# Optimization experiments

Measured on AMD Instinct MI355X. Metric: run time of the kernel, lower is better.

The kernel has to match this reference:

```python
import jax, jax.numpy as jnp
import numpy as np


def setup_inputs() -> dict:
    key = jax.random.key(0)
    k1, k2 = jax.random.split(key)
    N1, N2, C, W, H = 128, 128, 768, 16, 16
    x = jax.random.normal(k1, (N1, C, W, H), dtype=jnp.float32)
    y = jax.random.normal(k2, (N2, C, W, H), dtype=jnp.float32)
    return {"x": x, "y": y}


def reference(x, y):
    """NNGPKernel.forward with y given, diag=False, and the abstract
    propagate() taken as identity. Computes the initial ConvKP tensors:
      xy[n1*N2+n2, 0, w, h] = mean_c x[n1,c,w,h] * y[n2,c,w,h]
      xx[n1, 0, w, h]       = mean_c x[n1,c,w,h]**2
      yy[n2, 0, w, h]       = mean_c y[n2,c,w,h]**2
    The pairwise channel-mean is expressed as a batched contraction over c
    (per spatial location), avoiding the O(N1*N2*C*W*H) broadcast intermediate
    of the original torch code.
    """
    N1, C, W, H = x.shape
    N2 = y.shape[0]
    inv_c = jnp.asarray(1.0 / C, dtype=x.dtype)
    # [N1, N2, W, H] pairwise channel correlation, then flatten pair dims
    xy = (jnp.einsum('ncwh,mcwh->nmwh', x, y) * inv_c).reshape(N1 * N2, 1, W, H)
    xx = jnp.mean(x * x, axis=1, keepdims=True)  # [N1, 1, W, H]
    yy = jnp.mean(y * y, axis=1, keepdims=True)  # [N2, 1, W, H]
    return xy, xx, yy
```

## Files before the change

### kernel.cpp

```cpp
#include <hip/hip_runtime.h>

#define AS1 __attribute__((address_space(1)))
#define AS3 __attribute__((address_space(3)))

typedef float f32x4 __attribute__((ext_vector_type(4)));
typedef long lx2 __attribute__((ext_vector_type(2)));

static constexpr int C = 768;
static constexpr int NB = 128;
static constexpr int S  = 256;
static constexpr int XY_ELEMS  = NB * NB * S;
static constexpr int XSQ_ELEMS = NB * S;
static constexpr size_t WS_TENSOR_B = (size_t)S * NB * C;

__global__ __launch_bounds__(256) void pass1(const float* __restrict__ x,
                                             const float* __restrict__ y,
                                             unsigned char* __restrict__ xb,
                                             unsigned char* __restrict__ yb,
                                             float* __restrict__ out) {
  const int b      = blockIdx.x;
  const int tensor = b >> 10;
  const int local  = b & 1023;
  const int n      = local >> 3;
  const int st     = (local >> 1) & 3;
  const int ch2    = local & 1;

  const float*   src = tensor ? y  : x;
  unsigned char* dst = tensor ? yb : xb;
  float*         sqo = out + XY_ELEMS + tensor * XSQ_ELEMS;

  __shared__ float tile[2][32 * 68];

  const int t  = threadIdx.x;
  const int cl = t >> 4;
  const int s4 = (t & 15) * 4;
  const int sl = t >> 2;
  const int cq = t & 3;
  const int sn = (n >> 1) & 3;

  const float* srcn =
      src + (size_t)n * (C * S) + (size_t)(ch2 * 384) * S + st * 64;
  unsigned char* dstrow = dst + ((size_t)(st * 64 + sl) * NB + n) * C;

  f32x4 acc = {0.f, 0.f, 0.f, 0.f};
  f32x4 c0r, c1r, n0r, n1r;

  c0r = __builtin_nontemporal_load(
      reinterpret_cast<const f32x4*>(srcn + (size_t)cl * S + s4));
  c1r = __builtin_nontemporal_load(
      reinterpret_cast<const f32x4*>(srcn + (size_t)(16 + cl) * S + s4));

#pragma unroll
  for (int ch = 0; ch < 12; ++ch) {
    float* tb = tile[ch & 1];

    if (ch < 11) {
      const float* p0 = srcn + (size_t)((ch + 1) * 32 + cl) * S + s4;
      const float* p1 = srcn + (size_t)((ch + 1) * 32 + 16 + cl) * S + s4;
      n0r = __builtin_nontemporal_load(reinterpret_cast<const f32x4*>(p0));
      n1r = __builtin_nontemporal_load(reinterpret_cast<const f32x4*>(p1));
    }

    acc += c0r * c0r;
    acc += c1r * c1r;
    *reinterpret_cast<f32x4*>(
        &tb[cl * 68 + (s4 ^ (((cl >> 3) & 3) << 3))]) = c0r;
    *reinterpret_cast<f32x4*>(
        &tb[(16 + cl) * 68 + (s4 ^ ((((16 + cl) >> 3) & 3) << 3))]) = c1r;

    asm volatile("s_waitcnt lgkmcnt(0)" ::: "memory");
    __builtin_amdgcn_s_barrier();

    float f[8];
#pragma unroll
    for (int i = 0; i < 8; ++i)
      f[i] = tb[(cq * 8 + i) * 68 + (sl ^ (cq << 3))];
    int lo = __builtin_amdgcn_cvt_pk_fp8_f32(f[0], f[1], 0, false);
    lo     = __builtin_amdgcn_cvt_pk_fp8_f32(f[2], f[3], lo, true);
    int hi = __builtin_amdgcn_cvt_pk_fp8_f32(f[4], f[5], 0, false);
    hi     = __builtin_amdgcn_cvt_pk_fp8_f32(f[6], f[7], hi, true);
    uint2 v8 = make_uint2((unsigned)lo, (unsigned)hi);

    const int kt   = ch2 * 6 + (ch >> 1);
    const int slot = 2 * (cq ^ sn) + (ch & 1);
    *reinterpret_cast<uint2*>(dstrow + kt * 64 + slot * 8) = v8;

    c0r = n0r;
    c1r = n1r;
  }

  __syncthreads();
  float* part = &tile[0][0];
#pragma unroll
  for (int j = 0; j < 4; ++j) part[cl * 64 + s4 + j] = acc[j];
  __syncthreads();
  if (t < 64) {
    float ssum = 0.f;
#pragma unroll
    for (int i = 0; i < 16; ++i) ssum += part[i * 64 + t];
    atomicAdd(&sqo[n * S + st * 64 + t], ssum * (1.0f / 768.0f));
  }
}

__global__ __launch_bounds__(256) void pass2(const unsigned char* __restrict__ xb,
                                             const unsigned char* __restrict__ yb,
                                             float* __restrict__ ws2) {
  const int bid = blockIdx.x;
  const int s = ((bid & 7) << 5) | (bid >> 3);

  const unsigned char* A = xb + (size_t)s * (NB * C);
  const unsigned char* B = yb + (size_t)s * (NB * C);

  __shared__ unsigned char As[2][128 * 64];
  __shared__ unsigned char Bs[2][128 * 64];

  const int t    = threadIdx.x;
  const int lane = t & 63;
  const int w    = t >> 6;
  const int wn   = w >> 1;
  const int wm   = w & 1;

  const unsigned char* gA[2];
  const unsigned char* gB[2];
  int lo16[2];
#pragma unroll
  for (int i = 0; i < 2; ++i) {
    int ci  = i * 256 + t;
    int row = ci >> 2;
    int j16 = ci & 3;
    gA[i]   = A + row * C + j16 * 16;
    gB[i]   = B + row * C + j16 * 16;
    lo16[i] = ci * 16;
  }

#define STAGE(K0, BUF)                                                        \
  {                                                                           \
    _Pragma("unroll") for (int i = 0; i < 2; ++i) {                           \
      __builtin_amdgcn_global_load_lds(                                       \
          (const AS1 unsigned int*)(gA[i] + (K0)*64),                         \
          (AS3 unsigned int*)((char*)As[BUF] + lo16[i]), 16, 0, 0);           \
      __builtin_amdgcn_global_load_lds(                                       \
          (const AS1 unsigned int*)(gB[i] + (K0)*64),                         \
          (AS3 unsigned int*)((char*)Bs[BUF] + lo16[i]), 16, 0, 0);           \
    }                                                                         \
  }

  f32x4 acc[4][4] = {};

  STAGE(0, 0);

#pragma unroll
  for (int k0 = 0; k0 < 12; ++k0) {
    if (k0 < 11) STAGE(k0 + 1, (k0 + 1) & 1);

    if (k0 < 11) {
      asm volatile("s_waitcnt vmcnt(4)" ::: "memory");
    } else {
      asm volatile("s_waitcnt vmcnt(0)" ::: "memory");
    }
    __builtin_amdgcn_s_barrier();

    const char* Ab = (const char*)As[k0 & 1];
    const char* Bb = (const char*)Bs[k0 & 1];

    lx2 av[4], bv[4];
    const int q = lane >> 4;
#pragma unroll
    for (int mi = 0; mi < 4; ++mi) {
      int row = wn * 64 + mi * 16 + (lane & 15);
      av[mi] = *reinterpret_cast<const lx2*>(
          Ab + row * 64 + ((q ^ ((row >> 1) & 3)) * 16));
    }
#pragma unroll
    for (int nj = 0; nj < 4; ++nj) {
      int row = wm * 64 + nj * 16 + (lane & 15);
      bv[nj] = *reinterpret_cast<const lx2*>(
          Bb + row * 64 + ((q ^ ((row >> 1) & 3)) * 16));
    }
#pragma unroll
    for (int mi = 0; mi < 4; ++mi)
#pragma unroll
      for (int nj = 0; nj < 4; ++nj) {
        acc[mi][nj] = __builtin_amdgcn_mfma_f32_16x16x32_fp8_fp8(
            av[mi][0], bv[nj][0], acc[mi][nj], 0, 0, 0);
        acc[mi][nj] = __builtin_amdgcn_mfma_f32_16x16x32_fp8_fp8(
            av[mi][1], bv[nj][1], acc[mi][nj], 0, 0, 0);
      }

    if (k0 < 11) __builtin_amdgcn_s_barrier();
  }
#undef STAGE

  const float inv = 1.0f / 768.0f;
  float* w2 = ws2 + (size_t)s * (NB * NB);
#pragma unroll
  for (int mi = 0; mi < 4; ++mi) {
#pragma unroll
    for (int nj = 0; nj < 4; ++nj) {
      f32x4 v = acc[mi][nj] * inv;
      int mm = wm * 64 + nj * 16 + (lane & 15);
      int nn = wn * 64 + mi * 16 + (lane >> 4) * 4;
      *reinterpret_cast<f32x4*>(w2 + (size_t)mm * NB + nn) = v;
    }
  }
}

__global__ __launch_bounds__(256) void pass3(const float* __restrict__ ws2,
                                             float* __restrict__ out) {
  const int bid = blockIdx.x;
  const int m   = bid & 127;
  const int st  = (bid >> 7) & 3;
  const int nt  = bid >> 9;
  const int t   = threadIdx.x;
  const int l16 = t & 15;
  const int hi4 = t >> 4;

  __shared__ float tile[64 * 64];

  const float* src = ws2 + ((size_t)(st * 64) * NB + m) * NB + nt * 64;
#pragma unroll
  for (int i = 0; i < 4; ++i) {
    int s_local = hi4 + 16 * i;
    f32x4 v = *reinterpret_cast<const f32x4*>(
        src + (size_t)s_local * (NB * NB) + l16 * 4);
    int chunk = l16 ^ ((s_local >> 2) & 15);
    *reinterpret_cast<f32x4*>(&tile[s_local * 64 + chunk * 4]) = v;
  }
  __syncthreads();

  float* dst = out + ((size_t)(nt * 64) * NB + m) * S + st * 64;
#pragma unroll
  for (int i = 0; i < 4; ++i) {
    int n_local = hi4 + 16 * i;
    int cb      = (n_local >> 2) & 15;
    int ne      = n_local & 3;
    int s4      = l16 * 4;
    f32x4 v;
#pragma unroll
    for (int j = 0; j < 4; ++j) {
      int ss = s4 + j;
      v[j] = tile[ss * 64 + ((cb ^ ((ss >> 2) & 15)) << 2) + ne];
    }
    __builtin_nontemporal_store(
        v, reinterpret_cast<f32x4*>(dst + (size_t)n_local * (NB * S) + s4));
  }
}

extern "C" void kernel_launch(void* const* d_in, const int* in_sizes, int n_in,
                              void* d_out, int out_size, void* d_ws, size_t ws_size,
                              hipStream_t stream) {
  const float* x = (const float*)d_in[0];
  const float* y = (const float*)d_in[1];
  float* out = (float*)d_out;

  unsigned char* xb = (unsigned char*)d_ws;
  unsigned char* yb = xb + WS_TENSOR_B;
  float* ws2 = (float*)((char*)d_ws + 2 * WS_TENSOR_B);

  hipMemsetAsync(out + XY_ELEMS, 0, (size_t)2 * XSQ_ELEMS * sizeof(float),
                 stream);
  pass1<<<2048, 256, 0, stream>>>(x, y, xb, yb, out);
  pass2<<<256, 256, 0, stream>>>(xb, yb, ws2);
  pass3<<<1024, 256, 0, stream>>>(ws2, out);
}
```

Baseline: 84.04 us.

## Restructure fp8 quantize pass to full-row spatial tiles with per-thread square sums

Rewrites the first pass so each block covers all 256 spatial positions of a 128-channel slice, with one thread per spatial location. Each thread reads 16 channels per step from shared memory, accumulates the squared-sum itself, and writes 16 bytes of fp8. This removes the cross-thread partial-sum reduction and its extra barriers, and each block issues one atomic per spatial location per channel chunk. The cost is a grid of 1536 blocks instead of 2048, more loads in flight per thread, and unpadded shared-memory tiles whose column reads could hit bank conflicts.

```diff
diff --git a/kernel.cpp b/kernel.cpp
--- a/kernel.cpp
+++ b/kernel.cpp
@@ -19,87 +19,82 @@
                                              unsigned char* __restrict__ yb,
                                              float* __restrict__ out) {
   const int b      = blockIdx.x;
-  const int tensor = b >> 10;
-  const int local  = b & 1023;
-  const int n      = local >> 3;
-  const int st     = (local >> 1) & 3;
-  const int ch2    = local & 1;
+  const int tensor = b / 768;
+  const int local  = b - tensor * 768;
+  const int n      = local / 6;
+  const int cr     = local - n * 6;
 
   const float*   src = tensor ? y  : x;
   unsigned char* dst = tensor ? yb : xb;
   float*         sqo = out + XY_ELEMS + tensor * XSQ_ELEMS;
 
-  __shared__ float tile[2][32 * 68];
-
-  const int t  = threadIdx.x;
-  const int cl = t >> 4;
-  const int s4 = (t & 15) * 4;
-  const int sl = t >> 2;
-  const int cq = t & 3;
-  const int sn = (n >> 1) & 3;
-
-  const float* srcn =
-      src + (size_t)n * (C * S) + (size_t)(ch2 * 384) * S + st * 64;
-  unsigned char* dstrow = dst + ((size_t)(st * 64 + sl) * NB + n) * C;
-
-  f32x4 acc = {0.f, 0.f, 0.f, 0.f};
-  f32x4 c0r, c1r, n0r, n1r;
-
-  c0r = __builtin_nontemporal_load(
-      reinterpret_cast<const f32x4*>(srcn + (size_t)cl * S + s4));
-  c1r = __builtin_nontemporal_load(
-      reinterpret_cast<const f32x4*>(srcn + (size_t)(16 + cl) * S + s4));
-
-#pragma unroll
-  for (int ch = 0; ch < 12; ++ch) {
+  __shared__ float tile[2][16 * 256];
+
+  const int t    = threadIdx.x;
+  const int w    = t >> 6;
+  const int lane = t & 63;
+  const int sn   = (n >> 1) & 3;
+
+  const float* srcn = src + (size_t)n * (C * S) + (size_t)(cr * 128) * S;
+  unsigned char* dstrow = dst + ((size_t)t * NB + n) * C;
+
+  float sq = 0.f;
+  f32x4 cur[4], nxt[4];
+
+#pragma unroll
+  for (int i = 0; i < 4; ++i)
+    cur[i] = __builtin_nontemporal_load(reinterpret_cast<const f32x4*>(
+        srcn + (size_t)(i * 4 + w) * S + lane * 4));
+
+#pragma unroll
+  for (int ch = 0; ch < 8; ++ch) {
     float* tb = tile[ch & 1];
 
-    if (ch < 11) {
-      const float* p0 = srcn + (size_t)((ch + 1) * 32 + cl) * S + s4;
-      const float* p1 = srcn + (size_t)((ch + 1) * 32 + 16 + cl) * S + s4;
-      n0r = __builtin_nontemporal_load(reinterpret_cast<const f32x4*>(p0));
-      n1r = __builtin_nontemporal_load(reinterpret_cast<const f32x4*>(p1));
-    }
-
-    acc += c0r * c0r;
-    acc += c1r * c1r;
-    *reinterpret_cast<f32x4*>(
-        &tb[cl * 68 + (s4 ^ (((cl >> 3) & 3) << 3))]) = c0r;
-    *reinterpret_cast<f32x4*>(
-        &tb[(16 + cl) * 68 + (s4 ^ ((((16 + cl) >> 3) & 3) << 3))]) = c1r;
+    if (ch < 7) {
+#pragma unroll
+      for (int i = 0; i < 4; ++i)
+        nxt[i] = __builtin_nontemporal_load(reinterpret_cast<const f32x4*>(
+            srcn + (size_t)((ch + 1) * 16 + i * 4 + w) * S + lane * 4));
+    }
+
+#pragma unroll
+    for (int i = 0; i < 4; ++i)
+      *reinterpret_cast<f32x4*>(&tb[(i * 4 + w) * 256 + lane * 4]) = cur[i];
 
     asm volatile("s_waitcnt lgkmcnt(0)" ::: "memory");
     __builtin_amdgcn_s_barrier();
 
-    float f[8];
-#pragma unroll
-    for (int i = 0; i < 8; ++i)
-      f[i] = tb[(cq * 8 + i) * 68 + (sl ^ (cq << 3))];
-    int lo = __builtin_amdgcn_cvt_pk_fp8_f32(f[0], f[1], 0, false);
-    lo     = __builtin_amdgcn_cvt_pk_fp8_f32(f[2], f[3], lo, true);
-    int hi = __builtin_amdgcn_cvt_pk_fp8_f32(f[4], f[5], 0, false);
-    hi     = __builtin_amdgcn_cvt_pk_fp8_f32(f[6], f[7], hi, true);
-    uint2 v8 = make_uint2((unsigned)lo, (unsigned)hi);
-
-    const int kt   = ch2 * 6 + (ch >> 1);
-    const int slot = 2 * (cq ^ sn) + (ch & 1);
-    *reinterpret_cast<uint2*>(dstrow + kt * 64 + slot * 8) = v8;
-
-    c0r = n0r;
-    c1r = n1r;
-  }
-
-  __syncthreads();
-  float* part = &tile[0][0];
-#pragma unroll
-  for (int j = 0; j < 4; ++j) part[cl * 64 + s4 + j] = acc[j];
-  __syncthreads();
-  if (t < 64) {
-    float ssum = 0.f;
-#pragma unroll
-    for (int i = 0; i < 16; ++i) ssum += part[i * 64 + t];
-    atomicAdd(&sqo[n * S + st * 64 + t], ssum * (1.0f / 768.0f));
-  }
+    float f[16];
+#pragma unroll
+    for (int i = 0; i < 16; ++i) f[i] = tb[i * 256 + t];
+#pragma unroll
+    for (int i = 0; i < 16; ++i) sq += f[i] * f[i];
+
+    int w0 = __builtin_amdgcn_cvt_pk_fp8_f32(f[0], f[1], 0, false);
+    w0     = __builtin_amdgcn_cvt_pk_fp8_f32(f[2], f[3], w0, true);
+    int w1 = __builtin_amdgcn_cvt_pk_fp8_f32(f[4], f[5], 0, false);
+    w1     = __builtin_amdgcn_cvt_pk_fp8_f32(f[6], f[7], w1, true);
+    int w2 = __builtin_amdgcn_cvt_pk_fp8_f32(f[8], f[9], 0, false);
+    w2     = __builtin_amdgcn_cvt_pk_fp8_f32(f[10], f[11], w2, true);
+    int w3 = __builtin_amdgcn_cvt_pk_fp8_f32(f[12], f[13], 0, false);
+    w3     = __builtin_amdgcn_cvt_pk_fp8_f32(f[14], f[15], w3, true);
+
+    const int c0 = cr * 128 + ch * 16;
+    const int kt = c0 >> 6;
+    const int u0 = (c0 >> 3) & 7;
+    const int s0 = 2 * ((u0 & 3) ^ sn) + (u0 >> 2);
+    const int u1 = u0 + 1;
+    const int s1 = 2 * ((u1 & 3) ^ sn) + (u1 >> 2);
+    *reinterpret_cast<uint2*>(dstrow + kt * 64 + s0 * 8) =
+        make_uint2((unsigned)w0, (unsigned)w1);
+    *reinterpret_cast<uint2*>(dstrow + kt * 64 + s1 * 8) =
+        make_uint2((unsigned)w2, (unsigned)w3);
+
+#pragma unroll
+    for (int i = 0; i < 4; ++i) cur[i] = nxt[i];
+  }
+
+  atomicAdd(&sqo[n * S + t], sq * (1.0f / 768.0f));
 }
 
 __global__ __launch_bounds__(256) void pass2(const unsigned char* __restrict__ xb,
@@ -259,7 +254,7 @@
 
   hipMemsetAsync(out + XY_ELEMS, 0, (size_t)2 * XSQ_ELEMS * sizeof(float),
                  stream);
-  pass1<<<2048, 256, 0, stream>>>(x, y, xb, yb, out);
+  pass1<<<1536, 256, 0, stream>>>(x, y, xb, yb, out);
   pass2<<<256, 256, 0, stream>>>(xb, yb, ws2);
   pass3<<<1024, 256, 0, stream>>>(ws2, out);
 }
```

Result: slower. 105.3 us (+25.4%).
